# Optimization experiments

Measured on AMD Instinct MI355X. Metric: run time of the kernel, lower is better.

Reference implementation:

```python
import jax, jax.numpy as jnp
import numpy as np

WS = 7
NH = 12
DIM = 384
HD = DIM // NH
EPS = 1e-5


def _rel_index(ws):
    coords = np.stack(np.meshgrid(np.arange(ws), np.arange(ws), indexing='ij'))
    cf = coords.transpose(1, 2, 0).reshape(-1, 2)  # [N,2]
    rel = cf[:, None, :] - cf[None, :, :]
    rel[:, :, 0] += ws - 1
    rel[:, :, 1] += ws - 1
    rel[:, :, 0] *= 2 * ws - 1
    return rel.sum(-1).astype(np.int32)  # [N,N]


def setup_inputs() -> dict:
    key = jax.random.key(0)
    ks = jax.random.split(key, 12)
    B, H, W, C = 32, 56, 56, DIM
    hid = 4 * C
    s = 0.02
    return {
        'x': jax.random.normal(ks[0], (B, H, W, C), jnp.float32),
        'ln1_g': jnp.ones((C,), jnp.float32),
        'ln1_b': jnp.zeros((C,), jnp.float32),
        'qkv_w': jax.random.normal(ks[1], (C, 3 * C), jnp.float32) * s,
        'qkv_b': jnp.zeros((3 * C,), jnp.float32),
        'bias_table': jax.random.normal(ks[2], ((2 * WS - 1) ** 2, NH), jnp.float32) * s,
        'proj_w': jax.random.normal(ks[3], (C, C), jnp.float32) * s,
        'proj_b': jnp.zeros((C,), jnp.float32),
        'ln2_g': jnp.ones((C,), jnp.float32),
        'ln2_b': jnp.zeros((C,), jnp.float32),
        'mlp_w1': jax.random.normal(ks[4], (C, hid), jnp.float32) * s,
        'mlp_b1': jnp.zeros((hid,), jnp.float32),
        'mlp_w2': jax.random.normal(ks[5], (hid, C), jnp.float32) * s,
        'mlp_b2': jnp.zeros((C,), jnp.float32),
        'rel_index': jnp.asarray(_rel_index(WS)),  # int32 [49,49]
    }


def _ln(x, g, b):
    m = jnp.mean(x, -1, keepdims=True)
    v = jnp.mean(jnp.square(x - m), -1, keepdims=True)
    return (x - m) * jax.lax.rsqrt(v + EPS) * g + b


def reference(x, ln1_g, ln1_b, qkv_w, qkv_b, bias_table, proj_w, proj_b,
              ln2_g, ln2_b, mlp_w1, mlp_b1, mlp_w2, mlp_b2, rel_index):
    B, H, W, C = x.shape
    N = WS * WS
    # norm1 + window partition: (B,H,W,C) -> (B*nW, N, C)
    xn = _ln(x, ln1_g, ln1_b)
    xw = xn.reshape(B, H // WS, WS, W // WS, WS, C).transpose(0, 1, 3, 2, 4, 5)
    xw = xw.reshape(-1, N, C)
    # qkv
    qkv = xw @ qkv_w + qkv_b  # [Bw, N, 3C]
    qkv = qkv.reshape(-1, N, 3, NH, HD).transpose(2, 0, 3, 1, 4)  # [3,Bw,nh,N,hd]
    q, k, v = qkv[0], qkv[1], qkv[2]
    attn = jnp.einsum('bhnd,bhmd->bhnm', q, k) * (HD ** -0.5)
    # relative position bias: gather [N*N] -> [N,N,nh] -> [nh,N,N]
    bias = bias_table[rel_index.reshape(-1)].reshape(N, N, NH).transpose(2, 0, 1)
    attn = jax.nn.softmax(attn + bias[None], axis=-1)
    out = jnp.einsum('bhnm,bhmd->bhnd', attn, v).transpose(0, 2, 1, 3).reshape(-1, N, C)
    out = out @ proj_w + proj_b
    # unpartition
    out = out.reshape(B, H // WS, W // WS, WS, WS, C).transpose(0, 1, 3, 2, 4, 5)
    out = out.reshape(B, H, W, C)
    x = x + out
    # MLP
    h = jax.nn.gelu(_ln(x, ln2_g, ln2_b) @ mlp_w1 + mlp_b1, approximate=False)
    x = x + (h @ mlp_w2 + mlp_b2)
    return x
```

## Files before the change

### kernel.cpp

```cpp
#include <hip/hip_runtime.h>
#include <cstdint>
#include <cmath>


typedef unsigned short US;
typedef __attribute__((ext_vector_type(4))) float f32x4;
typedef __attribute__((ext_vector_type(8))) __bf16 bf16x8;
typedef __attribute__((ext_vector_type(8))) US u16x8;
typedef __attribute__((ext_vector_type(4))) US u16x4;

__device__ __forceinline__ float bf2f(US u) {
  unsigned int i = ((unsigned int)u) << 16;
  float f;
  __builtin_memcpy(&f, &i, 4);
  return f;
}
__device__ __forceinline__ US f2bf(float f) {
  unsigned int i;
  __builtin_memcpy(&i, &f, 4);
  unsigned int lsb = (i >> 16) & 1u;
  i += 0x7fffu + lsb;
  return (US)(i >> 16);
}
__device__ __forceinline__ float ldin(const US* p, long i, bool f32) {
  return f32 ? ((const float*)p)[i] : bf2f(p[i]);
}
__device__ __forceinline__ bool probe_f32(const US* probe) {
  return probe[0] == 0;
}

__device__ __forceinline__ int pix2win(int p) {
  int b = p / 3136;
  int rem = p - b * 3136;
  int y = rem / 56;
  int x = rem - y * 56;
  return ((b * 8 + y / 7) * 8 + x / 7) * 49 + (y % 7) * 7 + (x % 7);
}
__device__ __forceinline__ int win2pix(int r) {
  int bw = r / 49;
  int t  = r - bw * 49;
  int b  = bw >> 6;
  int hw = (bw >> 3) & 7;
  int ww = bw & 7;
  int i  = t / 7;
  int j  = t - i * 7;
  return b * 3136 + (hw * 7 + i) * 56 + (ww * 7 + j);
}

__device__ __forceinline__ void gload16(const US* g, US* l) {
  __builtin_amdgcn_global_load_lds(
      (const __attribute__((address_space(1))) unsigned int*)g,
      (__attribute__((address_space(3))) unsigned int*)l, 16, 0, 0);
}
__device__ __forceinline__ bf16x8 frag_ld(const US* p, bool valid) {
  u16x8 r = valid ? *(const u16x8*)p : (u16x8){0, 0, 0, 0, 0, 0, 0, 0};
  bf16x8 f;
  __builtin_memcpy(&f, &r, 16);
  return f;
}

__global__ __launch_bounds__(256)
void transp(const US* __restrict__ in, US* __restrict__ out, int K, int N,
            const US* __restrict__ probe) {
  const bool f32 = probe_f32(probe);
  const long idx = (long)blockIdx.x * 256 + threadIdx.x;
  if (idx >= (long)K * N) return;
  const int n = (int)(idx % N);
  const int k = (int)(idx / N);
  out[(long)n * K + k] = f32 ? f2bf(((const float*)in)[idx]) : in[idx];
}

__global__ __launch_bounds__(256)
void bias_pre(const US* __restrict__ btab, const int* __restrict__ relidx,
              US* __restrict__ bp, const US* __restrict__ probe) {
  const bool f32 = probe_f32(probe);
  const int idx = blockIdx.x * 256 + threadIdx.x;
  const int h = idx >> 12;
  const int j = (idx >> 6) & 63;
  const int i = idx & 63;
  float v;
  if (j < 49) v = (i < 49) ? ldin(btab, (long)relidx[i * 49 + j] * 12 + h, f32) : 0.f;
  else v = -1e30f;
  bp[idx] = f2bf(v);
}

__global__ __launch_bounds__(256)
void ln_part(const US* __restrict__ x, const US* __restrict__ g,
             const US* __restrict__ b, US* __restrict__ y, int permute,
             const US* __restrict__ probe, int x_is_bf16) {
  const bool f32 = x_is_bf16 ? false : probe_f32(probe);
  const bool f32s = probe_f32(probe);
  const int p = blockIdx.x * 4 + (threadIdx.x >> 6);
  const int lane = threadIdx.x & 63;
  const long rb = (long)p * 384;
  float v[6];
  float s = 0.f;
#pragma unroll
  for (int r = 0; r < 6; r++) { v[r] = ldin(x, rb + lane + (r << 6), f32); s += v[r]; }
#pragma unroll
  for (int o = 1; o < 64; o <<= 1) s += __shfl_xor(s, o);
  const float mean = s * (1.f / 384.f);
  float q = 0.f;
#pragma unroll
  for (int r = 0; r < 6; r++) { float d = v[r] - mean; q += d * d; }
#pragma unroll
  for (int o = 1; o < 64; o <<= 1) q += __shfl_xor(q, o);
  const float rstd = rsqrtf(q * (1.f / 384.f) + 1e-5f);
  const long orow = permute ? (long)pix2win(p) : (long)p;
  US* yr = y + orow * 384;
#pragma unroll
  for (int r = 0; r < 6; r++) {
    const int c = lane + (r << 6);
    yr[c] = f2bf((v[r] - mean) * rstd * ldin(g, c, f32s) + ldin(b, c, f32s));
  }
}

template <int EPI>
__global__ __launch_bounds__(256, 3)
void gemm_bf16(const US* __restrict__ A, const US* __restrict__ BT,
               const US* __restrict__ bias, const US* __restrict__ res,
               US* __restrict__ out, int M, int N, int K,
               const US* __restrict__ probe) {
  (void)M;
  const bool f32 = probe_f32(probe);
  __shared__ __align__(16) US Ls[3][2][64 * 64];

  const int tid  = threadIdx.x;
  const int lane = tid & 63;
  const int wm   = (tid >> 6) >> 1;
  const int wn   = (tid >> 6) & 1;
  const int l15  = lane & 15;
  const int g    = lane >> 4;

  const int nCol = gridDim.y;
  const int nwg  = (int)(gridDim.x * gridDim.y);
  const int orig = blockIdx.y * gridDim.x + blockIdx.x;
  const int wi   = (orig & 7) * (nwg >> 3) + (orig >> 3);
  const int mBlk = wi / nCol;
  const int nBlk = wi - mBlk * nCol;
  const long bmBase = (long)mBlk * 128;
  const long bnBase = (long)nBlk * 128;

  const int r1 = tid >> 3;
  const int sl = (tid & 7) ^ (r1 & 7);
  const int tr = r1 + ((sl >> 2) << 6);
  const int ke = (sl & 3) << 3;
  const US* aS = A  + (bmBase + tr) * (long)K + ke;
  const US* bS = BT + (bnBase + tr) * (long)K + ke;
  const long r32 = (long)32 * K;

  auto stage = [&](int buf, int k0) {
    US* la = &Ls[buf][0][tid * 8];
    US* lb = &Ls[buf][1][tid * 8];
    gload16(aS + k0, la);
    gload16(aS + k0 + r32, la + 2048);
    gload16(bS + k0, lb);
    gload16(bS + k0 + r32, lb + 2048);
  };

  f32x4 acc[4][4];
#pragma unroll
  for (int i = 0; i < 4; i++)
#pragma unroll
    for (int j = 0; j < 4; j++) acc[i][j] = (f32x4){0.f, 0.f, 0.f, 0.f};

  const int l7   = l15 & 7;
  const int baseA = l15 * 64 + ((((wm << 2) | g) ^ l7) << 3);
  const int baseB = l15 * 64 + ((((wn << 2) | g) ^ l7) << 3);

  const int nT = K >> 5;
  stage(0, 0);
  stage(1, 32);
  int cur = 0, sb = 2;
  for (int t = 0; t < nT; ++t) {
    if (t + 1 < nT) asm volatile("s_waitcnt vmcnt(4)" ::: "memory");
    else            asm volatile("s_waitcnt vmcnt(0)" ::: "memory");
    __builtin_amdgcn_s_barrier();
    if (t + 2 < nT) {
      stage(sb, (t + 2) << 5);
      sb = (sb == 2) ? 0 : sb + 1;
    }
    __builtin_amdgcn_sched_barrier(0);

    const US* LA = &Ls[cur][0][0];
    const US* LB = &Ls[cur][1][0];
    bf16x8 af[4], bfv[4];
#pragma unroll
    for (int mi = 0; mi < 4; mi++)
      af[mi] = *(const bf16x8*)&LA[baseA + mi * 1024];
#pragma unroll
    for (int ni = 0; ni < 4; ni++)
      bfv[ni] = *(const bf16x8*)&LB[baseB + ni * 1024];
#pragma unroll
    for (int mi = 0; mi < 4; mi++)
#pragma unroll
      for (int ni = 0; ni < 4; ni++)
        acc[mi][ni] = __builtin_amdgcn_mfma_f32_16x16x32_bf16(
            af[mi], bfv[ni], acc[mi][ni], 0, 0, 0);
    cur = (cur == 2) ? 0 : cur + 1;
  }

  US* Cs = &Ls[0][0][0];
  __syncthreads();
  {
    const int rloc = (wm << 6) + (g << 2);
    const int cloc = (wn << 6) + l15;
#pragma unroll
    for (int ni = 0; ni < 4; ni++) {
      const int col = (int)bnBase + cloc + ni * 16;
      const float bv = ldin(bias, col, f32);
#pragma unroll
      for (int mi = 0; mi < 4; mi++) {
#pragma unroll
        for (int t = 0; t < 4; t++) {
          float v = acc[mi][ni][t] + bv;
          if (EPI == 2) v = 0.5f * v * (1.0f + erff(v * 0.70710678118654752f));
          Cs[(rloc + mi * 16 + t) * 128 + cloc + ni * 16] = f2bf(v);
        }
      }
    }
  }
  __syncthreads();
  const int cg  = tid & 15;
  const int rw0 = tid >> 4;
#pragma unroll
  for (int p = 0; p < 8; p++) {
    const int rl  = p * 16 + rw0;
    const int row = (int)bmBase + rl;
    long orow = row;
    if (EPI == 1) orow = win2pix(row);
    const int col = (int)bnBase + (cg << 3);
    const u16x8 hv = *(const u16x8*)&Cs[rl * 128 + (cg << 3)];
    const long oi = orow * (long)N + col;
    if (EPI == 0 || EPI == 2) {
      *(u16x8*)&out[oi] = hv;
    } else if (EPI == 1) {
      u16x8 o;
      if (f32) {
        const float* rp = (const float*)res + oi;
        f32x4 r0 = *(const f32x4*)rp;
        f32x4 r1 = *(const f32x4*)(rp + 4);
#pragma unroll
        for (int e = 0; e < 4; e++) o[e] = f2bf(bf2f(hv[e]) + r0[e]);
#pragma unroll
        for (int e = 0; e < 4; e++) o[e + 4] = f2bf(bf2f(hv[e + 4]) + r1[e]);
      } else {
        const u16x8 rv = *(const u16x8*)&res[oi];
#pragma unroll
        for (int e = 0; e < 8; e++) o[e] = f2bf(bf2f(hv[e]) + bf2f(rv[e]));
      }
      *(u16x8*)&out[oi] = o;
    } else {
      const u16x8 rv = *(const u16x8*)&res[oi];
      if (f32) {
        f32x4 o0, o1;
#pragma unroll
        for (int e = 0; e < 4; e++) o0[e] = bf2f(hv[e]) + bf2f(rv[e]);
#pragma unroll
        for (int e = 0; e < 4; e++) o1[e] = bf2f(hv[e + 4]) + bf2f(rv[e + 4]);
        float* op = (float*)out + oi;
        *(f32x4*)op = o0;
        *(f32x4*)(op + 4) = o1;
      } else {
        u16x8 o;
#pragma unroll
        for (int e = 0; e < 8; e++) o[e] = f2bf(bf2f(hv[e]) + bf2f(rv[e]));
        *(u16x8*)&out[oi] = o;
      }
    }
  }
}

__global__ __launch_bounds__(128)
void attn_win(const US* __restrict__ qkv, const US* __restrict__ bp,
              US* __restrict__ out) {
  const int w    = blockIdx.x;
  const int wave = threadIdx.x >> 6;
  const int h    = blockIdx.y * 2 + wave;
  const int lane = threadIdx.x & 63;
  const int l15  = lane & 15;
  const int g    = lane >> 4;
  const int g8   = g << 3;

  __shared__ __align__(16) US Ps[2][64 * 72];
  __shared__ __align__(16) US Vt[2][32 * 72];
  US* PsW = Ps[wave];
  US* VtW = Vt[wave];

  const US* base = qkv + (long)w * 49 * 1152 + h * 32;

  bf16x8 qa[4], kb[4];
#pragma unroll
  for (int mi = 0; mi < 4; mi++) {
    const int i = l15 + mi * 16;
    qa[mi] = frag_ld(base + (long)i * 1152 + g8, i < 49);
  }
#pragma unroll
  for (int ni = 0; ni < 4; ni++) {
    const int j = l15 + ni * 16;
    kb[ni] = frag_ld(base + (long)j * 1152 + 384 + g8, j < 49);
  }

  {
    const int j = lane;
    u16x8 rv[4];
    if (j < 49) {
      const US* vp = base + (long)j * 1152 + 768;
#pragma unroll
      for (int c = 0; c < 4; c++) rv[c] = *(const u16x8*)(vp + c * 8);
    } else {
#pragma unroll
      for (int c = 0; c < 4; c++) rv[c] = (u16x8){0, 0, 0, 0, 0, 0, 0, 0};
    }
#pragma unroll
    for (int c = 0; c < 4; c++)
#pragma unroll
      for (int d = 0; d < 8; d++) VtW[(c * 8 + d) * 72 + j] = rv[c][d];
  }

  f32x4 acc[4][4];
#pragma unroll
  for (int i = 0; i < 4; i++)
#pragma unroll
    for (int j = 0; j < 4; j++) acc[i][j] = (f32x4){0.f, 0.f, 0.f, 0.f};
#pragma unroll
  for (int mi = 0; mi < 4; mi++)
#pragma unroll
    for (int ni = 0; ni < 4; ni++)
      acc[mi][ni] = __builtin_amdgcn_mfma_f32_16x16x32_bf16(
          qa[mi], kb[ni], acc[mi][ni], 0, 0, 0);

  u16x4 bias4[4][4];
#pragma unroll
  for (int mi = 0; mi < 4; mi++)
#pragma unroll
    for (int ni = 0; ni < 4; ni++)
      bias4[mi][ni] = *(const u16x4*)&bp[(long)h * 4096 +
                                         (long)(l15 + ni * 16) * 64 +
                                         mi * 16 + g * 4];

  const float scale = 0.17677669529663687f;
#pragma unroll
  for (int mi = 0; mi < 4; mi++)
#pragma unroll
    for (int t = 0; t < 4; t++) {
      float v0 = acc[mi][0][t] * scale + bf2f(bias4[mi][0][t]);
      float v1 = acc[mi][1][t] * scale + bf2f(bias4[mi][1][t]);
      float v2 = acc[mi][2][t] * scale + bf2f(bias4[mi][2][t]);
      float v3 = acc[mi][3][t] * scale + bf2f(bias4[mi][3][t]);
      float m = fmaxf(fmaxf(v0, v1), fmaxf(v2, v3));
      m = fmaxf(m, __shfl_xor(m, 1));
      m = fmaxf(m, __shfl_xor(m, 2));
      m = fmaxf(m, __shfl_xor(m, 4));
      m = fmaxf(m, __shfl_xor(m, 8));
      float e0 = __expf(v0 - m), e1 = __expf(v1 - m);
      float e2 = __expf(v2 - m), e3 = __expf(v3 - m);
      float sum = (e0 + e1) + (e2 + e3);
      sum += __shfl_xor(sum, 1);
      sum += __shfl_xor(sum, 2);
      sum += __shfl_xor(sum, 4);
      sum += __shfl_xor(sum, 8);
      const float inv = 1.f / sum;
      acc[mi][0][t] = e0 * inv;
      acc[mi][1][t] = e1 * inv;
      acc[mi][2][t] = e2 * inv;
      acc[mi][3][t] = e3 * inv;
    }

#pragma unroll
  for (int mi = 0; mi < 4; mi++)
#pragma unroll
    for (int t = 0; t < 4; t++)
#pragma unroll
      for (int ni = 0; ni < 4; ni++)
        PsW[(mi * 16 + g * 4 + t) * 72 + l15 + ni * 16] = f2bf(acc[mi][ni][t]);

  __syncthreads();

  f32x4 acc2[2][4];
#pragma unroll
  for (int i = 0; i < 2; i++)
#pragma unroll
    for (int j = 0; j < 4; j++) acc2[i][j] = (f32x4){0.f, 0.f, 0.f, 0.f};
#pragma unroll
  for (int kk2 = 0; kk2 < 2; kk2++) {
    bf16x8 va[2], pb[4];
#pragma unroll
    for (int mi = 0; mi < 2; mi++)
      va[mi] = frag_ld(&VtW[(l15 + mi * 16) * 72 + kk2 * 32 + g8], true);
#pragma unroll
    for (int ni = 0; ni < 4; ni++)
      pb[ni] = frag_ld(&PsW[(l15 + ni * 16) * 72 + kk2 * 32 + g8], true);
#pragma unroll
    for (int mi = 0; mi < 2; mi++)
#pragma unroll
      for (int ni = 0; ni < 4; ni++)
        acc2[mi][ni] = __builtin_amdgcn_mfma_f32_16x16x32_bf16(
            va[mi], pb[ni], acc2[mi][ni], 0, 0, 0);
  }

#pragma unroll
  for (int ni = 0; ni < 4; ni++) {
    const int i = l15 + ni * 16;
    if (i < 49) {
#pragma unroll
      for (int mi = 0; mi < 2; mi++) {
        u16x4 o;
#pragma unroll
        for (int t = 0; t < 4; t++) o[t] = f2bf(acc2[mi][ni][t]);
        *(u16x4*)&out[((long)w * 49 + i) * 384 + h * 32 + mi * 16 + g * 4] = o;
      }
    }
  }
}

extern "C" void kernel_launch(void* const* d_in, const int* in_sizes, int n_in,
                              void* d_out, int out_size, void* d_ws,
                              size_t ws_size, hipStream_t stream) {
  (void)in_sizes; (void)n_in; (void)out_size;
  const US* x      = (const US*)d_in[0];
  const US* ln1_g  = (const US*)d_in[1];
  const US* ln1_b  = (const US*)d_in[2];
  const US* qkv_w  = (const US*)d_in[3];
  const US* qkv_b  = (const US*)d_in[4];
  const US* btab   = (const US*)d_in[5];
  const US* proj_w = (const US*)d_in[6];
  const US* proj_b = (const US*)d_in[7];
  const US* ln2_g  = (const US*)d_in[8];
  const US* ln2_b  = (const US*)d_in[9];
  const US* mlp_w1 = (const US*)d_in[10];
  const US* mlp_b1 = (const US*)d_in[11];
  const US* mlp_w2 = (const US*)d_in[12];
  const US* mlp_b2 = (const US*)d_in[13];
  const int* relidx = (const int*)d_in[14];
  US* out = (US*)d_out;
  const US* probe = ln1_g;

  if (ws_size < 465960960u) return;
  char* ws = (char*)d_ws;
  US* qkvwT  = (US*)(ws + 0);
  US* projwT = (US*)(ws + 884736);
  US* w1T    = (US*)(ws + 1179648);
  US* w2T    = (US*)(ws + 2359296);
  US* regA   = (US*)(ws + 3538944);
  US* regB   = (US*)(ws + 80609280);
  US* biasP  = (US*)(ws + 311820288);
  US* x1     = (US*)(ws + 388890624);

  transp<<<1728, 256, 0, stream>>>(qkv_w, qkvwT, 384, 1152, probe);
  transp<<<576,  256, 0, stream>>>(proj_w, projwT, 384, 384, probe);
  transp<<<2304, 256, 0, stream>>>(mlp_w1, w1T, 384, 1536, probe);
  transp<<<2304, 256, 0, stream>>>(mlp_w2, w2T, 1536, 384, probe);
  bias_pre<<<192, 256, 0, stream>>>(btab, relidx, biasP, probe);

  ln_part<<<25088, 256, 0, stream>>>(x, ln1_g, ln1_b, regA, 1, probe, 0);

  gemm_bf16<0><<<dim3(784, 9), 256, 0, stream>>>(regA, qkvwT, qkv_b, nullptr,
                                                 regB, 100352, 1152, 384, probe);

  attn_win<<<dim3(2048, 6), 128, 0, stream>>>(regB, biasP, regA);

  gemm_bf16<1><<<dim3(784, 3), 256, 0, stream>>>(regA, projwT, proj_b, x, x1,
                                                 100352, 384, 384, probe);

  ln_part<<<25088, 256, 0, stream>>>(x1, ln2_g, ln2_b, regA, 0, probe, 1);

  gemm_bf16<2><<<dim3(784, 12), 256, 0, stream>>>(regA, w1T, mlp_b1, nullptr,
                                                  regB, 100352, 1536, 384, probe);

  gemm_bf16<3><<<dim3(784, 3), 256, 0, stream>>>(regB, w2T, mlp_b2, x1, out,
                                                 100352, 384, 1536, probe);
}
```

Before: 1.111 ms.

## Fuse LayerNorm2, MLP FC1, GELU and FC2 into a single kernel

Measured after the change: 1.317 ms. 1.19x slower.

```diff
diff --git a/kernel.cpp b/kernel.cpp
--- a/kernel.cpp
+++ b/kernel.cpp
@@ -57,6 +57,9 @@
   bf16x8 f;
   __builtin_memcpy(&f, &r, 16);
   return f;
+}
+__device__ __forceinline__ f32x4 mfma16(bf16x8 a, bf16x8 b, f32x4 c) {
+  return __builtin_amdgcn_mfma_f32_16x16x32_bf16(a, b, c, 0, 0, 0);
 }
 
 __global__ __launch_bounds__(256)
@@ -195,8 +198,7 @@
     for (int mi = 0; mi < 4; mi++)
 #pragma unroll
       for (int ni = 0; ni < 4; ni++)
-        acc[mi][ni] = __builtin_amdgcn_mfma_f32_16x16x32_bf16(
-            af[mi], bfv[ni], acc[mi][ni], 0, 0, 0);
+        acc[mi][ni] = mfma16(af[mi], bfv[ni], acc[mi][ni]);
     cur = (cur == 2) ? 0 : cur + 1;
   }
 
@@ -214,7 +216,6 @@
 #pragma unroll
         for (int t = 0; t < 4; t++) {
           float v = acc[mi][ni][t] + bv;
-          if (EPI == 2) v = 0.5f * v * (1.0f + erff(v * 0.70710678118654752f));
           Cs[(rloc + mi * 16 + t) * 128 + cloc + ni * 16] = f2bf(v);
         }
       }
@@ -232,9 +233,9 @@
     const int col = (int)bnBase + (cg << 3);
     const u16x8 hv = *(const u16x8*)&Cs[rl * 128 + (cg << 3)];
     const long oi = orow * (long)N + col;
-    if (EPI == 0 || EPI == 2) {
+    if (EPI == 0) {
       *(u16x8*)&out[oi] = hv;
-    } else if (EPI == 1) {
+    } else {
       u16x8 o;
       if (f32) {
         const float* rp = (const float*)res + oi;
@@ -250,23 +251,184 @@
         for (int e = 0; e < 8; e++) o[e] = f2bf(bf2f(hv[e]) + bf2f(rv[e]));
       }
       *(u16x8*)&out[oi] = o;
+    }
+  }
+}
+
+__global__ __launch_bounds__(512, 2)
+void fused_mlp(const US* __restrict__ x1, const US* __restrict__ w1T,
+               const US* __restrict__ w2T, const US* __restrict__ lng,
+               const US* __restrict__ lnb, const US* __restrict__ b1,
+               const US* __restrict__ b2, US* __restrict__ out,
+               const US* __restrict__ probe) {
+  const bool f32 = probe_f32(probe);
+  __shared__ __align__(16) US U[57344];
+  US* const B1 = U;
+  US* const B2 = U + 16384;
+  US* const HS = U + 40960;
+
+  const int tid  = threadIdx.x;
+  const int wv   = tid >> 6;
+  const int lane = tid & 63;
+  const int l15  = lane & 15;
+  const int g    = lane >> 4;
+  const int l7   = l15 & 7;
+  const long bmBase = (long)blockIdx.x * 128;
+
+  const int r1b = tid >> 3;
+  const int sl1 = (tid & 7) ^ (r1b & 7);
+  const US* w1s = w1T + (long)r1b * 384 + sl1 * 8;
+  const int r2b = tid >> 2;
+  const int sl2 = (tid & 3) ^ ((r2b ^ (r2b >> 2)) & 3);
+  const US* w2s = w2T + (long)r2b * 1536 + sl2 * 8;
+
+  const int pb1a = l15 * 64 + ((g ^ l7) << 3);
+  const int pb1b = l15 * 64 + (((4 + g) ^ l7) << 3);
+  const int xl   = (l15 ^ (l15 >> 2)) & 3;
+  const int pb2  = l15 * 32 + ((g ^ xl) << 3);
+  US* const hw   = HS + wv * 2048;
+
+  auto stageB1 = [&](int buf, int j, int kc2) {
+    US* d = B1 + buf * 8192 + tid * 8;
+    const US* s = w1s + (long)(j * 128) * 384 + kc2 * 64;
+    gload16(s, d);
+    gload16(s + (long)64 * 384, d + 4096);
+  };
+  auto stageB2 = [&](int buf, int j, int kc) {
+    US* d = B2 + buf * 12288 + tid * 8;
+    const US* s = w2s + j * 128 + kc * 32;
+    gload16(s, d);
+    gload16(s + (long)128 * 1536, d + 4096);
+    gload16(s + (long)256 * 1536, d + 8192);
+  };
+
+  stageB1(0, 0, 0);
+
+  const long rowg = bmBase + wv * 16 + l15;
+  u16x8 raw[12];
+#pragma unroll
+  for (int kc = 0; kc < 12; kc++)
+    raw[kc] = *(const u16x8*)&x1[rowg * 384 + kc * 32 + g * 8];
+  float s = 0.f;
+#pragma unroll
+  for (int kc = 0; kc < 12; kc++)
+#pragma unroll
+    for (int e = 0; e < 8; e++) s += bf2f(raw[kc][e]);
+  s += __shfl_xor(s, 16);
+  s += __shfl_xor(s, 32);
+  const float mean = s * (1.f / 384.f);
+  float q = 0.f;
+#pragma unroll
+  for (int kc = 0; kc < 12; kc++)
+#pragma unroll
+    for (int e = 0; e < 8; e++) { float d = bf2f(raw[kc][e]) - mean; q += d * d; }
+  q += __shfl_xor(q, 16);
+  q += __shfl_xor(q, 32);
+  const float rstd = rsqrtf(q * (1.f / 384.f) + 1e-5f);
+  bf16x8 A1[12];
+#pragma unroll
+  for (int kc = 0; kc < 12; kc++) {
+    u16x8 tv;
+#pragma unroll
+    for (int e = 0; e < 8; e++) {
+      const int c = kc * 32 + g * 8 + e;
+      tv[e] = f2bf((bf2f(raw[kc][e]) - mean) * rstd * ldin(lng, c, f32) +
+                   ldin(lnb, c, f32));
+    }
+    __builtin_memcpy(&A1[kc], &tv, 16);
+  }
+
+  f32x4 oac[24];
+#pragma unroll
+  for (int i = 0; i < 24; i++) oac[i] = (f32x4){0.f, 0.f, 0.f, 0.f};
+
+  for (int j = 0; j < 12; j++) {
+    f32x4 hac[8];
+#pragma unroll
+    for (int i = 0; i < 8; i++) hac[i] = (f32x4){0.f, 0.f, 0.f, 0.f};
+
+    for (int kc2 = 0; kc2 < 6; kc2++) {
+      asm volatile("s_waitcnt vmcnt(0)" ::: "memory");
+      __builtin_amdgcn_s_barrier();
+      __builtin_amdgcn_sched_barrier(0);
+      if (kc2 < 5) stageB1((kc2 + 1) & 1, j, kc2 + 1);
+      else         stageB2(0, j, 0);
+      const US* bp = B1 + (kc2 & 1) * 8192;
+      const bf16x8 a0 = A1[kc2 * 2];
+      const bf16x8 a1 = A1[kc2 * 2 + 1];
+#pragma unroll
+      for (int ni = 0; ni < 8; ni++) {
+        bf16x8 bf0 = *(const bf16x8*)&bp[ni * 1024 + pb1a];
+        hac[ni] = mfma16(a0, bf0, hac[ni]);
+      }
+#pragma unroll
+      for (int ni = 0; ni < 8; ni++) {
+        bf16x8 bf1 = *(const bf16x8*)&bp[ni * 1024 + pb1b];
+        hac[ni] = mfma16(a1, bf1, hac[ni]);
+      }
+    }
+
+#pragma unroll
+    for (int ni = 0; ni < 8; ni++) {
+      const float bv = ldin(b1, j * 128 + ni * 16 + l15, f32);
+#pragma unroll
+      for (int t = 0; t < 4; t++) {
+        float v = hac[ni][t] + bv;
+        v = 0.5f * v * (1.0f + erff(v * 0.70710678118654752f));
+        const int rr = g * 4 + t;
+        hw[rr * 128 + (((ni * 2 + (l15 >> 3)) ^ (rr & 7)) << 3) + l7] = f2bf(v);
+      }
+    }
+
+    for (int kc = 0; kc < 4; kc++) {
+      asm volatile("s_waitcnt vmcnt(0)" ::: "memory");
+      __builtin_amdgcn_s_barrier();
+      __builtin_amdgcn_sched_barrier(0);
+      if (kc < 3)       stageB2((kc + 1) & 1, j, kc + 1);
+      else if (j < 11)  stageB1(0, j + 1, 0);
+      const US* bp = B2 + (kc & 1) * 12288;
+      const bf16x8 a2 =
+          *(const bf16x8*)&hw[l15 * 128 + ((((kc << 2) | g) ^ l7) << 3)];
+#pragma unroll
+      for (int ni = 0; ni < 24; ni++) {
+        bf16x8 bf = *(const bf16x8*)&bp[ni * 512 + pb2];
+        oac[ni] = mfma16(a2, bf, oac[ni]);
+      }
+    }
+  }
+
+  __builtin_amdgcn_s_barrier();
+  US* const Cs = U;
+#pragma unroll
+  for (int ni = 0; ni < 24; ni++) {
+    const float bv = ldin(b2, ni * 16 + l15, f32);
+#pragma unroll
+    for (int t = 0; t < 4; t++)
+      Cs[(wv * 16 + g * 4 + t) * 384 + ni * 16 + l15] = f2bf(oac[ni][t] + bv);
+  }
+  __syncthreads();
+#pragma unroll
+  for (int p = 0; p < 12; p++) {
+    const int id  = p * 512 + tid;
+    const int row = id / 48;
+    const int col = (id - row * 48) * 8;
+    const u16x8 hv = *(const u16x8*)&Cs[row * 384 + col];
+    const long oi = (bmBase + row) * 384 + col;
+    const u16x8 rv = *(const u16x8*)&x1[oi];
+    if (f32) {
+      f32x4 o0, o1;
+#pragma unroll
+      for (int e = 0; e < 4; e++) o0[e] = bf2f(hv[e]) + bf2f(rv[e]);
+#pragma unroll
+      for (int e = 0; e < 4; e++) o1[e] = bf2f(hv[e + 4]) + bf2f(rv[e + 4]);
+      float* op = (float*)out + oi;
+      *(f32x4*)op = o0;
+      *(f32x4*)(op + 4) = o1;
     } else {
-      const u16x8 rv = *(const u16x8*)&res[oi];
-      if (f32) {
-        f32x4 o0, o1;
-#pragma unroll
-        for (int e = 0; e < 4; e++) o0[e] = bf2f(hv[e]) + bf2f(rv[e]);
-#pragma unroll
-        for (int e = 0; e < 4; e++) o1[e] = bf2f(hv[e + 4]) + bf2f(rv[e + 4]);
-        float* op = (float*)out + oi;
-        *(f32x4*)op = o0;
-        *(f32x4*)(op + 4) = o1;
-      } else {
-        u16x8 o;
-#pragma unroll
-        for (int e = 0; e < 8; e++) o[e] = f2bf(bf2f(hv[e]) + bf2f(rv[e]));
-        *(u16x8*)&out[oi] = o;
-      }
+      u16x8 o;
+#pragma unroll
+      for (int e = 0; e < 8; e++) o[e] = f2bf(bf2f(hv[e]) + bf2f(rv[e]));
+      *(u16x8*)&out[oi] = o;
     }
   }
 }
@@ -327,8 +489,7 @@
   for (int mi = 0; mi < 4; mi++)
 #pragma unroll
     for (int ni = 0; ni < 4; ni++)
-      acc[mi][ni] = __builtin_amdgcn_mfma_f32_16x16x32_bf16(
-          qa[mi], kb[ni], acc[mi][ni], 0, 0, 0);
+      acc[mi][ni] = mfma16(qa[mi], kb[ni], acc[mi][ni]);
 
   u16x4 bias4[4][4];
 #pragma unroll
@@ -395,8 +556,7 @@
     for (int mi = 0; mi < 2; mi++)
 #pragma unroll
       for (int ni = 0; ni < 4; ni++)
-        acc2[mi][ni] = __builtin_amdgcn_mfma_f32_16x16x32_bf16(
-            va[mi], pb[ni], acc2[mi][ni], 0, 0, 0);
+        acc2[mi][ni] = mfma16(va[mi], pb[ni], acc2[mi][ni]);
   }
 
 #pragma unroll
@@ -463,11 +623,6 @@
   gemm_bf16<1><<<dim3(784, 3), 256, 0, stream>>>(regA, projwT, proj_b, x, x1,
                                                  100352, 384, 384, probe);
 
-  ln_part<<<25088, 256, 0, stream>>>(x1, ln2_g, ln2_b, regA, 0, probe, 1);
-
-  gemm_bf16<2><<<dim3(784, 12), 256, 0, stream>>>(regA, w1T, mlp_b1, nullptr,
-                                                  regB, 100352, 1536, 384, probe);
-
-  gemm_bf16<3><<<dim3(784, 3), 256, 0, stream>>>(regB, w2T, mlp_b2, x1, out,
-                                                 100352, 384, 1536, probe);
-}
+  fused_mlp<<<784, 512, 0, stream>>>(x1, w1T, w2T, ln2_g, ln2_b,
+                                     mlp_b1, mlp_b2, out, probe);
+}
```
